# Kernel tuning notes

Hardware: AMD Instinct MI355X
Metric: run time of the kernel (lower is better)

Reference implementation:

```python
import jax, jax.numpy as jnp
import numpy as np

B = 4096
N = 4096
ORDER = 3


def setup_inputs() -> dict:
    key = jax.random.key(0)
    kx, kw, kb = jax.random.split(key, 3)
    x = jax.random.normal(kx, (B, N), dtype=jnp.float32)
    # xavier-uniform-like init for [order, n, 1] params (fan_in=n, fan_out=1)
    limit = float(np.sqrt(6.0 / (N + 1)))
    w = jax.random.uniform(kw, (ORDER, N, 1), dtype=jnp.float32, minval=-limit, maxval=limit)
    b = jax.random.uniform(kb, (ORDER, N, 1), dtype=jnp.float32, minval=-limit, maxval=limit)
    return {"x": x, "w": w, "b": b}


def reference(x, w, b):
    # Original per step i (with x, x_k as [B, n, 1] columns):
    #   temp = x @ x_k^T            -> [B, n, n]
    #   x_k  = temp @ w[i] + b[i] + x_k
    # By associativity: (x x_k^T) w[i] = x * (x_k . w[i]) — same math, O(B*n).
    order = w.shape[0]
    x_k = x  # [B, n]
    outs = []
    for i in range(order):
        s = x_k @ w[i, :, 0]                      # [B] = x_k^T w_i per sample
        x_k = x * s[:, None] + b[i, :, 0] + x_k   # [B, n]
        outs.append(x_k)
    return tuple(outs)
```

## Files before the change

### kernel.cpp

```cpp
#include <hip/hip_runtime.h>


constexpr int BLK = 256;

typedef float f32x4 __attribute__((ext_vector_type(4)));

__device__ __forceinline__ float dot4(f32x4 a, f32x4 b) {
    return a.x * b.x + a.y * b.y + a.z * b.z + a.w * b.w;
}

__global__ __launch_bounds__(BLK) void crossnet_fused(
    const float* __restrict__ x,
    const float* __restrict__ w,
    const float* __restrict__ b,
    float* __restrict__ out,
    int B, int N)
{
    const int row = blockIdx.x;
    const int tid = threadIdx.x;

    const size_t base = (size_t)row * N;
    const f32x4* x4 = (const f32x4*)(x + base);
    const f32x4* w0 = (const f32x4*)(w);
    const f32x4* w1 = (const f32x4*)(w + N);
    const f32x4* w2 = (const f32x4*)(w + 2 * (size_t)N);
    const f32x4* b0 = (const f32x4*)(b);
    const f32x4* b1 = (const f32x4*)(b + N);
    const f32x4* b2 = (const f32x4*)(b + 2 * (size_t)N);

    f32x4 xv[4];
    float p0 = 0.f, p1 = 0.f, p2 = 0.f;
    float q1 = 0.f, q2 = 0.f;

    #pragma unroll
    for (int c = 0; c < 4; ++c) {
        const int idx = c * BLK + tid;
        const f32x4 xx = x4[idx];
        const f32x4 wa = w0[idx];
        const f32x4 wb = w1[idx];
        const f32x4 wc = w2[idx];
        const f32x4 ba = b0[idx];
        const f32x4 bb = b1[idx];
        xv[c] = xx;
        p0 += dot4(xx, wa);
        p1 += dot4(xx, wb);
        p2 += dot4(xx, wc);
        q1 += dot4(ba, wb);
        q2 += dot4(ba + bb, wc);
    }

    #pragma unroll
    for (int off = 32; off > 0; off >>= 1) {
        p0 += __shfl_down(p0, off);
        p1 += __shfl_down(p1, off);
        p2 += __shfl_down(p2, off);
        q1 += __shfl_down(q1, off);
        q2 += __shfl_down(q2, off);
    }

    __shared__ float red[4][8];
    const int wave = tid >> 6, lane = tid & 63;
    if (lane == 0) {
        red[wave][0] = p0; red[wave][1] = p1; red[wave][2] = p2;
        red[wave][3] = q1; red[wave][4] = q2;
    }
    __syncthreads();

    const float u0 = red[0][0] + red[1][0] + red[2][0] + red[3][0];
    const float u1 = red[0][1] + red[1][1] + red[2][1] + red[3][1];
    const float u2 = red[0][2] + red[1][2] + red[2][2] + red[3][2];
    const float t1 = red[0][3] + red[1][3] + red[2][3] + red[3][3];
    const float t2 = red[0][4] + red[1][4] + red[2][4] + red[3][4];

    const float c1 = 1.0f + u0;
    const float s1 = c1 * u1 + t1;
    const float c2 = c1 + s1;
    const float s2 = c2 * u2 + t2;
    const float c3 = c2 + s2;

    f32x4* o0 = (f32x4*)(out + base);
    f32x4* o1 = (f32x4*)(out + (size_t)B * N + base);
    f32x4* o2 = (f32x4*)(out + 2 * (size_t)B * N + base);

    #pragma unroll
    for (int c = 0; c < 4; ++c) {
        const int idx = c * BLK + tid;
        const f32x4 ba = b0[idx];
        const f32x4 bb = b1[idx];
        const f32x4 bc = b2[idx];
        const f32x4 cb2 = ba + bb;
        const f32x4 cb3 = cb2 + bc;
        o0[idx] = xv[c] * c1 + ba;
        o1[idx] = xv[c] * c2 + cb2;
        o2[idx] = xv[c] * c3 + cb3;
    }
}

extern "C" void kernel_launch(void* const* d_in, const int* in_sizes, int n_in,
                              void* d_out, int out_size, void* d_ws, size_t ws_size,
                              hipStream_t stream) {
    const float* x = (const float*)d_in[0];
    const float* w = (const float*)d_in[1];
    const float* b = (const float*)d_in[2];
    float* out = (float*)d_out;

    const int N = in_sizes[1] / 3;
    const int B = in_sizes[0] / N;

    crossnet_fused<<<B, BLK, 0, stream>>>(x, w, b, out, B, N);
}
```

Measured before the change: 50.91 us.

## Make kernel persistent over rows, caching weights and bias sums in registers

Launches 512 blocks of 512 threads, each handling a contiguous range of rows, instead of one block per row. The w vectors, cumulative bias sums and the bias-weight dot products are loaded and computed once per block and kept in registers, removing per-row reloads of w and b. The next row of x is prefetched while the current outputs are stored, and a double-buffered shared reduction array lets one barrier per row suffice. The cost is fewer blocks in flight, higher register use, and reliance on B dividing evenly by 512.

```diff
diff --git a/kernel.cpp b/kernel.cpp
--- a/kernel.cpp
+++ b/kernel.cpp
@@ -1,7 +1,8 @@
 #include <hip/hip_runtime.h>
 
 
-constexpr int BLK = 256;
+constexpr int BLK = 512;
+constexpr int CHUNK = 2;
 
 typedef float f32x4 __attribute__((ext_vector_type(4)));
 
@@ -9,18 +10,18 @@
     return a.x * b.x + a.y * b.y + a.z * b.z + a.w * b.w;
 }
 
-__global__ __launch_bounds__(BLK) void crossnet_fused(
+__global__ __launch_bounds__(BLK) void crossnet_persist(
     const float* __restrict__ x,
     const float* __restrict__ w,
     const float* __restrict__ b,
     float* __restrict__ out,
-    int B, int N)
+    int B, int N, int rows_per_blk)
 {
-    const int row = blockIdx.x;
     const int tid = threadIdx.x;
+    const int wave = tid >> 6;
+    const int lane = tid & 63;
+    const int nwaves = BLK / 64;
 
-    const size_t base = (size_t)row * N;
-    const f32x4* x4 = (const f32x4*)(x + base);
     const f32x4* w0 = (const f32x4*)(w);
     const f32x4* w1 = (const f32x4*)(w + N);
     const f32x4* w2 = (const f32x4*)(w + 2 * (size_t)N);
@@ -28,71 +29,102 @@
     const f32x4* b1 = (const f32x4*)(b + N);
     const f32x4* b2 = (const f32x4*)(b + 2 * (size_t)N);
 
-    f32x4 xv[4];
-    float p0 = 0.f, p1 = 0.f, p2 = 0.f;
+    f32x4 wv0[CHUNK], wv1[CHUNK], wv2[CHUNK];
+    f32x4 cb1[CHUNK], cb2[CHUNK], cb3[CHUNK];
     float q1 = 0.f, q2 = 0.f;
 
     #pragma unroll
-    for (int c = 0; c < 4; ++c) {
+    for (int c = 0; c < CHUNK; ++c) {
         const int idx = c * BLK + tid;
-        const f32x4 xx = x4[idx];
-        const f32x4 wa = w0[idx];
-        const f32x4 wb = w1[idx];
-        const f32x4 wc = w2[idx];
+        wv0[c] = w0[idx];
+        wv1[c] = w1[idx];
+        wv2[c] = w2[idx];
         const f32x4 ba = b0[idx];
         const f32x4 bb = b1[idx];
-        xv[c] = xx;
-        p0 += dot4(xx, wa);
-        p1 += dot4(xx, wb);
-        p2 += dot4(xx, wc);
-        q1 += dot4(ba, wb);
-        q2 += dot4(ba + bb, wc);
+        const f32x4 bc = b2[idx];
+        cb1[c] = ba;
+        cb2[c] = ba + bb;
+        cb3[c] = cb2[c] + bc;
+        q1 += dot4(ba, wv1[c]);
+        q2 += dot4(cb2[c], wv2[c]);
     }
+
+    __shared__ float redq[BLK / 64][2];
+    __shared__ float red[2][BLK / 64][3];
 
     #pragma unroll
     for (int off = 32; off > 0; off >>= 1) {
-        p0 += __shfl_down(p0, off);
-        p1 += __shfl_down(p1, off);
-        p2 += __shfl_down(p2, off);
         q1 += __shfl_down(q1, off);
         q2 += __shfl_down(q2, off);
     }
+    if (lane == 0) { redq[wave][0] = q1; redq[wave][1] = q2; }
+    __syncthreads();
+    float t1 = 0.f, t2 = 0.f;
+    #pragma unroll
+    for (int wv = 0; wv < nwaves; ++wv) { t1 += redq[wv][0]; t2 += redq[wv][1]; }
 
-    __shared__ float red[4][8];
-    const int wave = tid >> 6, lane = tid & 63;
-    if (lane == 0) {
-        red[wave][0] = p0; red[wave][1] = p1; red[wave][2] = p2;
-        red[wave][3] = q1; red[wave][4] = q2;
+    const int row0 = blockIdx.x * rows_per_blk;
+
+    f32x4 xcur[CHUNK];
+    {
+        const f32x4* x4 = (const f32x4*)(x + (size_t)row0 * N);
+        #pragma unroll
+        for (int c = 0; c < CHUNK; ++c) xcur[c] = x4[c * BLK + tid];
     }
-    __syncthreads();
 
-    const float u0 = red[0][0] + red[1][0] + red[2][0] + red[3][0];
-    const float u1 = red[0][1] + red[1][1] + red[2][1] + red[3][1];
-    const float u2 = red[0][2] + red[1][2] + red[2][2] + red[3][2];
-    const float t1 = red[0][3] + red[1][3] + red[2][3] + red[3][3];
-    const float t2 = red[0][4] + red[1][4] + red[2][4] + red[3][4];
+    for (int r = 0; r < rows_per_blk; ++r) {
+        const size_t base = (size_t)(row0 + r) * N;
 
-    const float c1 = 1.0f + u0;
-    const float s1 = c1 * u1 + t1;
-    const float c2 = c1 + s1;
-    const float s2 = c2 * u2 + t2;
-    const float c3 = c2 + s2;
+        float p0 = 0.f, p1 = 0.f, p2 = 0.f;
+        #pragma unroll
+        for (int c = 0; c < CHUNK; ++c) {
+            p0 += dot4(xcur[c], wv0[c]);
+            p1 += dot4(xcur[c], wv1[c]);
+            p2 += dot4(xcur[c], wv2[c]);
+        }
+        #pragma unroll
+        for (int off = 32; off > 0; off >>= 1) {
+            p0 += __shfl_down(p0, off);
+            p1 += __shfl_down(p1, off);
+            p2 += __shfl_down(p2, off);
+        }
+        const int buf = r & 1;
+        if (lane == 0) {
+            red[buf][wave][0] = p0; red[buf][wave][1] = p1; red[buf][wave][2] = p2;
+        }
+        __syncthreads();
+        float u0 = 0.f, u1 = 0.f, u2 = 0.f;
+        #pragma unroll
+        for (int wv = 0; wv < nwaves; ++wv) {
+            u0 += red[buf][wv][0]; u1 += red[buf][wv][1]; u2 += red[buf][wv][2];
+        }
 
-    f32x4* o0 = (f32x4*)(out + base);
-    f32x4* o1 = (f32x4*)(out + (size_t)B * N + base);
-    f32x4* o2 = (f32x4*)(out + 2 * (size_t)B * N + base);
+        const float c1 = 1.0f + u0;
+        const float s1 = c1 * u1 + t1;
+        const float c2 = c1 + s1;
+        const float s2 = c2 * u2 + t2;
+        const float c3 = c2 + s2;
 
-    #pragma unroll
-    for (int c = 0; c < 4; ++c) {
-        const int idx = c * BLK + tid;
-        const f32x4 ba = b0[idx];
-        const f32x4 bb = b1[idx];
-        const f32x4 bc = b2[idx];
-        const f32x4 cb2 = ba + bb;
-        const f32x4 cb3 = cb2 + bc;
-        o0[idx] = xv[c] * c1 + ba;
-        o1[idx] = xv[c] * c2 + cb2;
-        o2[idx] = xv[c] * c3 + cb3;
+        f32x4 xnext[CHUNK];
+        if (r + 1 < rows_per_blk) {
+            const f32x4* xn = (const f32x4*)(x + base + N);
+            #pragma unroll
+            for (int c = 0; c < CHUNK; ++c) xnext[c] = xn[c * BLK + tid];
+        }
+
+        f32x4* o0 = (f32x4*)(out + base);
+        f32x4* o1 = (f32x4*)(out + (size_t)B * N + base);
+        f32x4* o2 = (f32x4*)(out + 2 * (size_t)B * N + base);
+        #pragma unroll
+        for (int c = 0; c < CHUNK; ++c) {
+            const int idx = c * BLK + tid;
+            o0[idx] = xcur[c] * c1 + cb1[c];
+            o1[idx] = xcur[c] * c2 + cb2[c];
+            o2[idx] = xcur[c] * c3 + cb3[c];
+        }
+
+        #pragma unroll
+        for (int c = 0; c < CHUNK; ++c) xcur[c] = xnext[c];
     }
 }
 
@@ -107,5 +139,8 @@
     const int N = in_sizes[1] / 3;
     const int B = in_sizes[0] / N;
 
-    crossnet_fused<<<B, BLK, 0, stream>>>(x, w, b, out, B, N);
+    const int nblocks = 512;
+    const int rows_per_blk = B / nblocks;
+
+    crossnet_persist<<<nblocks, BLK, 0, stream>>>(x, w, b, out, B, N, rows_per_blk);
 }
```

New measurement: 47.74 us. 6.2% less time.
